# Kernel optimization log

Measured on AMD Instinct MI355X. Metric: run time of the kernel, lower is better.

Reference implementation:

```python
import jax, jax.numpy as jnp
import numpy as np

N = 30000        # nodes
E = 480000       # edges (before self-loops)
F_IN = 1280      # input_features
HID = 64         # hidden_dim
HEADS = 4
C = 2 * HID      # per-head GAT out channels (hidden_dim*2)
NEG_SLOPE = 0.2  # GATConv default negative_slope
EPS = 1e-5       # BatchNorm1d eps


def setup_inputs() -> dict:
    key = jax.random.key(0)
    ks = jax.random.split(key, 8)
    x = jax.random.normal(ks[0], (N, F_IN), jnp.float32)
    edge_index = jax.random.randint(ks[1], (2, E), 0, N)
    edge_weight = jax.random.uniform(ks[2], (E,), jnp.float32)
    W_gat = jax.random.normal(ks[3], (F_IN, HEADS * C), jnp.float32) / np.sqrt(F_IN)
    att_src = jax.random.normal(ks[4], (HEADS, C), jnp.float32) * 0.1
    att_dst = jax.random.normal(ks[5], (HEADS, C), jnp.float32) * 0.1
    b_gat = jnp.zeros((HEADS * C,), jnp.float32)
    bn_gamma = jnp.ones((HEADS * C,), jnp.float32)
    bn_beta = jnp.zeros((HEADS * C,), jnp.float32)
    W_gcn = jax.random.normal(ks[6], (HEADS * C, HID), jnp.float32) / np.sqrt(HEADS * C)
    b_gcn = jnp.zeros((HID,), jnp.float32)
    return dict(x=x, edge_index=edge_index, edge_weight=edge_weight, W_gat=W_gat,
                att_src=att_src, att_dst=att_dst, b_gat=b_gat, bn_gamma=bn_gamma,
                bn_beta=bn_beta, W_gcn=W_gcn, b_gcn=b_gcn)


def _segment_softmax(logits, seg, num):
    m = jax.ops.segment_max(logits, seg, num_segments=num)
    e = jnp.exp(logits - m[seg])
    s = jax.ops.segment_sum(e, seg, num_segments=num)
    return e / (s[seg] + 1e-16)


def reference(x, edge_index, edge_weight, W_gat, att_src, att_dst, b_gat,
              bn_gamma, bn_beta, W_gcn, b_gcn):
    n = x.shape[0]
    loops = jnp.arange(n)
    src = jnp.concatenate([edge_index[0], loops])  # self-loops added by both convs
    dst = jnp.concatenate([edge_index[1], loops])

    # ---- GATConv(F_IN -> HEADS*C, heads=4, concat) ----
    # (edge_weight plays no role: GATConv has edge_dim=None so edge_attr is unused)
    h = (x @ W_gat).reshape(n, HEADS, C)                  # [N,H,C]
    a_src = jnp.einsum('nhc,hc->nh', h, att_src)          # [N,H]
    a_dst = jnp.einsum('nhc,hc->nh', h, att_dst)
    logits = jax.nn.leaky_relu(a_src[src] + a_dst[dst], NEG_SLOPE)  # [E+N,H]
    alpha = _segment_softmax(logits, dst, n)              # softmax over incoming edges
    msg = h[src] * alpha[:, :, None]                      # [E+N,H,C]
    out1 = jax.ops.segment_sum(msg, dst, num_segments=n).reshape(n, HEADS * C) + b_gat

    # ---- BatchNorm1d (training-mode batch stats) + ReLU ----
    mean = out1.mean(axis=0)
    var = out1.var(axis=0)
    xr = jax.nn.relu((out1 - mean) * jax.lax.rsqrt(var + EPS) * bn_gamma + bn_beta)

    # ---- GCNConv(HEADS*C -> HID) with edge_weight, self-loops weight 1 ----
    w = jnp.concatenate([edge_weight, jnp.ones((n,), edge_weight.dtype)])
    deg = jax.ops.segment_sum(w, dst, num_segments=n)
    dinv = jnp.where(deg > 0, jax.lax.rsqrt(deg), 0.0)
    norm = dinv[src] * w * dinv[dst]                      # D^-1/2 A D^-1/2
    h2 = xr @ W_gcn                                       # [N,HID]
    out = jax.ops.segment_sum(h2[src] * norm[:, None], dst, num_segments=n) + b_gcn
    return out
```

## Files before the change

### kernel.cpp

```cpp
#include <hip/hip_runtime.h>
#include <hip/hip_bf16.h>
#include <math.h>

#define N_NODES 30000
#define N_EDGES 480000
#define EE_TOT  510000
#define F_INK   1280
#define HC      512
#define C_PH    128
#define NHID    64

typedef __attribute__((ext_vector_type(8))) short bf16x8;
typedef __attribute__((ext_vector_type(4))) float f32x4;

__device__ inline float wred_max(float v){
  #pragma unroll
  for (int o = 32; o; o >>= 1) v = fmaxf(v, __shfl_xor(v, o));
  return v;
}
__device__ inline float wred_sum(float v){
  #pragma unroll
  for (int o = 32; o; o >>= 1) v += __shfl_xor(v, o);
  return v;
}

__device__ __forceinline__ unsigned short f2bf(float f){
  unsigned u = __float_as_uint(f);
  unsigned r = (u + 0x7FFFu + ((u >> 16) & 1u)) >> 16;
  return (unsigned short)r;
}
__device__ __forceinline__ float b2f(unsigned short s){
  return __uint_as_float((unsigned)s << 16);
}

__device__ __forceinline__ void gld16(const void* g, void* l){
  __builtin_amdgcn_global_load_lds((const __attribute__((address_space(1))) unsigned int*)g,
                                   (__attribute__((address_space(3))) unsigned int*)l, 16, 0, 0);
}

__global__ __launch_bounds__(256) void cvtx(const float* __restrict__ x,
                                            unsigned short* __restrict__ xb){
  size_t i = ((size_t)blockIdx.x * 256 + threadIdx.x) * 4;
  float4 v = *(const float4*)&x[i];
  ushort4 o;
  o.x = f2bf(v.x); o.y = f2bf(v.y); o.z = f2bf(v.z); o.w = f2bf(v.w);
  *(ushort4*)&xb[i] = o;
}

__global__ __launch_bounds__(256) void cvtw(const float* __restrict__ W,
                                            unsigned short* __restrict__ Wb){
  __shared__ float tile[32][33];
  int tx = threadIdx.x & 31, ty = threadIdx.x >> 5;
  int n0 = blockIdx.x * 32, k0 = blockIdx.y * 32;
  #pragma unroll
  for (int i = 0; i < 4; i++){
    int r = ty + i * 8;
    tile[r][tx] = W[(size_t)(k0 + r) * HC + n0 + tx];
  }
  __syncthreads();
  #pragma unroll
  for (int i = 0; i < 4; i++){
    int r = ty + i * 8;
    Wb[(size_t)(n0 + r) * F_INK + k0 + tx] = f2bf(tile[tx][r]);
  }
}

__global__ __launch_bounds__(256) void cvtw2(const float* __restrict__ W,
                                             unsigned short* __restrict__ Wb){
  __shared__ float tile[32][33];
  int tx = threadIdx.x & 31, ty = threadIdx.x >> 5;
  int n0 = blockIdx.x * 32, k0 = blockIdx.y * 32;
  #pragma unroll
  for (int i = 0; i < 4; i++){
    int r = ty + i * 8;
    tile[r][tx] = W[(size_t)(k0 + r) * NHID + n0 + tx];
  }
  __syncthreads();
  #pragma unroll
  for (int i = 0; i < 4; i++){
    int r = ty + i * 8;
    Wb[(size_t)(n0 + r) * HC + k0 + tx] = f2bf(tile[tx][r]);
  }
}

#define BM 128
#define BK 32
#define KTILES (F_INK / BK)
__global__ __launch_bounds__(256) void gemm1_mfma(const unsigned short* __restrict__ A,
                                                  const unsigned short* __restrict__ B,
                                                  unsigned short* __restrict__ C){
  __shared__ __align__(16) unsigned short Ab[2][BM * BK];
  __shared__ __align__(16) unsigned short Bb[2][BM * BK];
  const int t = threadIdx.x, lane = t & 63, wid = t >> 6;
  const int wm = wid >> 1, wn = wid & 1;
  const int bm = blockIdx.y * BM, bn = blockIdx.x * BM;
  const int r15 = lane & 15;
  const int kq  = (lane >> 4) * 16;
  const int kqs = kq ^ (((r15 >> 1) & 3) << 4);
  const int srow  = (lane >> 2);
  const int skb   = ((lane & 3) * 16) ^ (((lane >> 3) & 3) << 4);

  f32x4 acc[4][4] = {};

  auto stage = [&](int buf, int kt){
    const int k0 = kt * BK;
    #pragma unroll
    for (int c = 0; c < 2; c++){
      int chunk = wid * 2 + c;
      int row = chunk * 16 + srow;
      int ar = bm + row; if (ar >= N_NODES) ar = N_NODES - 1;
      gld16(&A[(size_t)ar * F_INK + k0 + (skb >> 1)], &Ab[buf][chunk * 512]);
      gld16(&B[(size_t)(bn + row) * F_INK + k0 + (skb >> 1)], &Bb[buf][chunk * 512]);
    }
  };

  stage(0, 0);
  __syncthreads();

  for (int kt = 0; kt < KTILES; kt++){
    const int cur = kt & 1;
    if (kt + 1 < KTILES) stage(cur ^ 1, kt + 1);
    bf16x8 a[4], b[4];
    #pragma unroll
    for (int f = 0; f < 4; f++){
      int rowA = wm * 64 + f * 16 + r15;
      a[f] = *(const bf16x8*)((const char*)&Ab[cur][0] + rowA * 64 + kqs);
      int rowB = wn * 64 + f * 16 + r15;
      b[f] = *(const bf16x8*)((const char*)&Bb[cur][0] + rowB * 64 + kqs);
    }
    #pragma unroll
    for (int fm = 0; fm < 4; fm++)
      #pragma unroll
      for (int fn = 0; fn < 4; fn++)
        acc[fm][fn] = __builtin_amdgcn_mfma_f32_16x16x32_bf16(a[fm], b[fn], acc[fm][fn], 0, 0, 0);
    __syncthreads();
  }

  const int ccol0 = bn + wn * 64 + r15;
  #pragma unroll
  for (int fm = 0; fm < 4; fm++){
    #pragma unroll
    for (int j = 0; j < 4; j++){
      int row = bm + wm * 64 + fm * 16 + (lane >> 4) * 4 + j;
      if (row < N_NODES){
        #pragma unroll
        for (int fn = 0; fn < 4; fn++)
          C[(size_t)row * HC + ccol0 + fn * 16] = f2bf(acc[fm][fn][j]);
      }
    }
  }
}

__global__ __launch_bounds__(256) void attdot(const unsigned short* __restrict__ hb,
    const float* __restrict__ att_s, const float* __restrict__ att_d,
    float* __restrict__ a_src, float* __restrict__ a_dst){
  int n = blockIdx.x;
  int w = threadIdx.x >> 6;
  int lane = threadIdx.x & 63;
  const unsigned short* hr = hb + (size_t)n * HC + w * C_PH;
  ushort2 hv = *(const ushort2*)(hr + 2 * lane);
  float h0 = b2f(hv.x), h1 = b2f(hv.y);
  const float* as = att_s + w * C_PH;
  const float* ad = att_d + w * C_PH;
  float s1 = h0 * as[2*lane] + h1 * as[2*lane + 1];
  float s2 = h0 * ad[2*lane] + h1 * ad[2*lane + 1];
  s1 = wred_sum(s1); s2 = wred_sum(s2);
  if (lane == 0){ a_src[n*4 + w] = s1; a_dst[n*4 + w] = s2; }
}

__global__ void count_k(const int* __restrict__ ei, int* __restrict__ counts){
  int e = blockIdx.x * 256 + threadIdx.x;
  if (e >= EE_TOT) return;
  int d = (e < N_EDGES) ? ei[N_EDGES + e] : (e - N_EDGES);
  atomicAdd(&counts[d], 1);
}

__global__ __launch_bounds__(1024) void scan_k(const int* __restrict__ counts,
                                               int* __restrict__ offsets){
  __shared__ int sh[1024];
  int t = threadIdx.x;
  int base = t * 30;
  int tot = 0;
  for (int i = 0; i < 30; i++){
    int idx = base + i;
    tot += (idx < N_NODES) ? counts[idx] : 0;
  }
  sh[t] = tot; __syncthreads();
  for (int o = 1; o < 1024; o <<= 1){
    int v = (t >= o) ? sh[t - o] : 0;
    __syncthreads();
    sh[t] += v;
    __syncthreads();
  }
  int run = sh[t] - tot;
  for (int i = 0; i < 30; i++){
    int idx = base + i;
    if (idx < N_NODES){ offsets[idx] = run; run += counts[idx]; }
  }
  if (t == 1023) offsets[N_NODES] = sh[1023];
}

__global__ void fill_k(const int* __restrict__ ei, const float* __restrict__ ew,
                       int* __restrict__ cursor, const int* __restrict__ offsets,
                       int* __restrict__ src_s, float* __restrict__ w_s){
  int e = blockIdx.x * 256 + threadIdx.x;
  if (e >= EE_TOT) return;
  int s, d; float w;
  if (e < N_EDGES){ s = ei[e]; d = ei[N_EDGES + e]; w = ew[e]; }
  else            { s = d = e - N_EDGES; w = 1.0f; }
  int pos = offsets[d] + atomicAdd(&cursor[d], 1);
  src_s[pos] = s; w_s[pos] = w;
}

__global__ __launch_bounds__(64) void attnprep(const int* __restrict__ offsets,
    const int* __restrict__ src_s, const float* __restrict__ w_s,
    const float* __restrict__ a_src, const float* __restrict__ a_dst,
    float* __restrict__ alpha, float* __restrict__ dinv){
  int n = blockIdx.x, lane = threadIdx.x;
  int off = offsets[n], end = offsets[n + 1];
  float4 ad = *(const float4*)&a_dst[n * 4];
  float m0 = -1e30f, m1 = -1e30f, m2 = -1e30f, m3 = -1e30f;
  for (int i = off + lane; i < end; i += 64){
    int s = src_s[i];
    float4 as = *(const float4*)&a_src[s * 4];
    float l0 = as.x + ad.x; l0 = (l0 > 0.f) ? l0 : 0.2f * l0;
    float l1 = as.y + ad.y; l1 = (l1 > 0.f) ? l1 : 0.2f * l1;
    float l2 = as.z + ad.z; l2 = (l2 > 0.f) ? l2 : 0.2f * l2;
    float l3 = as.w + ad.w; l3 = (l3 > 0.f) ? l3 : 0.2f * l3;
    m0 = fmaxf(m0, l0); m1 = fmaxf(m1, l1); m2 = fmaxf(m2, l2); m3 = fmaxf(m3, l3);
  }
  m0 = wred_max(m0); m1 = wred_max(m1); m2 = wred_max(m2); m3 = wred_max(m3);
  float s0 = 0, s1 = 0, s2 = 0, s3 = 0, wsum = 0;
  for (int i = off + lane; i < end; i += 64){
    int s = src_s[i];
    float4 as = *(const float4*)&a_src[s * 4];
    float l0 = as.x + ad.x; l0 = (l0 > 0.f) ? l0 : 0.2f * l0;
    float l1 = as.y + ad.y; l1 = (l1 > 0.f) ? l1 : 0.2f * l1;
    float l2 = as.z + ad.z; l2 = (l2 > 0.f) ? l2 : 0.2f * l2;
    float l3 = as.w + ad.w; l3 = (l3 > 0.f) ? l3 : 0.2f * l3;
    float e0 = expf(l0 - m0), e1 = expf(l1 - m1), e2 = expf(l2 - m2), e3 = expf(l3 - m3);
    float4 av; av.x = e0; av.y = e1; av.z = e2; av.w = e3;
    *(float4*)&alpha[(size_t)i * 4] = av;
    s0 += e0; s1 += e1; s2 += e2; s3 += e3;
    wsum += w_s[i];
  }
  s0 = wred_sum(s0); s1 = wred_sum(s1); s2 = wred_sum(s2); s3 = wred_sum(s3);
  wsum = wred_sum(wsum);
  if (lane == 0) dinv[n] = (wsum > 0.f) ? rsqrtf(wsum) : 0.f;
  float r0 = 1.f / (s0 + 1e-16f), r1 = 1.f / (s1 + 1e-16f);
  float r2 = 1.f / (s2 + 1e-16f), r3 = 1.f / (s3 + 1e-16f);
  for (int i = off + lane; i < end; i += 64){
    float4 av = *(float4*)&alpha[(size_t)i * 4];
    av.x *= r0; av.y *= r1; av.z *= r2; av.w *= r3;
    *(float4*)&alpha[(size_t)i * 4] = av;
  }
}

__global__ __launch_bounds__(256) void gatagg(const int* __restrict__ offsets,
    const int* __restrict__ src_s, const float* __restrict__ alpha,
    const unsigned short* __restrict__ hb, const float* __restrict__ b_gat,
    float* __restrict__ out1){
  __shared__ int   s_l[64];
  __shared__ float a_s[64][4];
  int n = blockIdx.x, t = threadIdx.x, wid = t >> 6;
  int off = offsets[n], deg = offsets[n + 1] - off;
  float acc0 = 0, acc1 = 0;
  for (int done = 0; done < deg; done += 64){
    int ce = deg - done; if (ce > 64) ce = 64;
    __syncthreads();
    if (t < 64 && t < ce){
      int idx = off + done + t;
      s_l[t] = src_s[idx];
      float4 av = *(const float4*)&alpha[(size_t)idx * 4];
      a_s[t][0] = av.x; a_s[t][1] = av.y; a_s[t][2] = av.z; a_s[t][3] = av.w;
    }
    __syncthreads();
    for (int i = 0; i < ce; i++){
      const ushort2* hp = (const ushort2*)(hb + (size_t)s_l[i] * HC);
      ushort2 hv = hp[t];
      float a = a_s[i][wid];
      acc0 += b2f(hv.x) * a;
      acc1 += b2f(hv.y) * a;
    }
  }
  float2 o; o.x = acc0 + b_gat[2*t]; o.y = acc1 + b_gat[2*t + 1];
  *(float2*)&out1[(size_t)n * HC + 2*t] = o;
}

__global__ __launch_bounds__(256) void bnstats(const float* __restrict__ out1,
                                               float* __restrict__ bnacc){
  int t = threadIdx.x;
  float s1 = 0, q1 = 0, s2 = 0, q2 = 0;
  for (int n = blockIdx.x; n < N_NODES; n += gridDim.x){
    float v1 = out1[(size_t)n * HC + t];
    float v2 = out1[(size_t)n * HC + t + 256];
    s1 += v1; q1 += v1 * v1; s2 += v2; q2 += v2 * v2;
  }
  atomicAdd(&bnacc[t], s1);        atomicAdd(&bnacc[512 + t], q1);
  atomicAdd(&bnacc[t + 256], s2);  atomicAdd(&bnacc[512 + t + 256], q2);
}

__global__ void bnfinal(const float* __restrict__ bnacc, const float* __restrict__ gam,
                        const float* __restrict__ bet, float* __restrict__ bnp){
  int c = blockIdx.x * 256 + threadIdx.x;
  if (c >= 512) return;
  float mean = bnacc[c] * (1.0f / N_NODES);
  float var  = bnacc[512 + c] * (1.0f / N_NODES) - mean * mean;
  float sc = gam[c] * rsqrtf(var + 1e-5f);
  bnp[c] = sc;
  bnp[512 + c] = bet[c] - mean * sc;
}

__global__ __launch_bounds__(256) void bnprep(const float* __restrict__ out1,
    const float* __restrict__ bnp, unsigned short* __restrict__ xrb){
  size_t i = ((size_t)blockIdx.x * 256 + threadIdx.x) * 4;
  int c = (int)(i & (HC - 1));
  float4 v  = *(const float4*)&out1[i];
  float4 sc = *(const float4*)&bnp[c];
  float4 sh = *(const float4*)&bnp[512 + c];
  float r; ushort4 o;
  r = v.x * sc.x + sh.x; o.x = f2bf(r > 0.f ? r : 0.f);
  r = v.y * sc.y + sh.y; o.y = f2bf(r > 0.f ? r : 0.f);
  r = v.z * sc.z + sh.z; o.z = f2bf(r > 0.f ? r : 0.f);
  r = v.w * sc.w + sh.w; o.w = f2bf(r > 0.f ? r : 0.f);
  *(ushort4*)&xrb[i] = o;
}

#define BM2 128
#define BK2 32
__global__ __launch_bounds__(256) void gemm2_mfma(const unsigned short* __restrict__ A,
                                                  const unsigned short* __restrict__ B,
                                                  float* __restrict__ C){
  __shared__ __align__(16) unsigned short Ab[2][BM2 * BK2];
  __shared__ __align__(16) unsigned short Bb[2][NHID * BK2];
  const int t = threadIdx.x, lane = t & 63, wid = t >> 6;
  const int bm = blockIdx.x * BM2;
  const int r15 = lane & 15;
  const int kq  = (lane >> 4) * 16;
  const int kqs = kq ^ (((r15 >> 1) & 3) << 4);
  const int srow = lane >> 2;
  const int skb  = ((lane & 3) * 16) ^ (((lane >> 3) & 3) << 4);

  f32x4 acc[2][4] = {};

  auto stage = [&](int buf, int kt){
    const int k0 = kt * BK2;
    #pragma unroll
    for (int c = 0; c < 2; c++){
      int chunk = wid * 2 + c;
      int row = chunk * 16 + srow;
      int ar = bm + row; if (ar >= N_NODES) ar = N_NODES - 1;
      gld16(&A[(size_t)ar * HC + k0 + (skb >> 1)], &Ab[buf][chunk * 512]);
    }
    int rowB = wid * 16 + srow;
    gld16(&B[(size_t)rowB * HC + k0 + (skb >> 1)], &Bb[buf][wid * 512]);
  };

  stage(0, 0);
  __syncthreads();

  #pragma unroll 2
  for (int kt = 0; kt < HC / BK2; kt++){
    const int cur = kt & 1;
    if (kt + 1 < HC / BK2) stage(cur ^ 1, kt + 1);
    bf16x8 a[2], b[4];
    #pragma unroll
    for (int f = 0; f < 2; f++){
      int rowA = wid * 32 + f * 16 + r15;
      a[f] = *(const bf16x8*)((const char*)&Ab[cur][0] + rowA * 64 + kqs);
    }
    #pragma unroll
    for (int f = 0; f < 4; f++){
      int rowB = f * 16 + r15;
      b[f] = *(const bf16x8*)((const char*)&Bb[cur][0] + rowB * 64 + kqs);
    }
    #pragma unroll
    for (int fm = 0; fm < 2; fm++)
      #pragma unroll
      for (int fn = 0; fn < 4; fn++)
        acc[fm][fn] = __builtin_amdgcn_mfma_f32_16x16x32_bf16(a[fm], b[fn], acc[fm][fn], 0, 0, 0);
    __syncthreads();
  }

  #pragma unroll
  for (int fm = 0; fm < 2; fm++){
    #pragma unroll
    for (int j = 0; j < 4; j++){
      int row = bm + wid * 32 + fm * 16 + (lane >> 4) * 4 + j;
      if (row < N_NODES){
        #pragma unroll
        for (int fn = 0; fn < 4; fn++)
          C[(size_t)row * NHID + fn * 16 + r15] = acc[fm][fn][j];
      }
    }
  }
}

__global__ __launch_bounds__(64) void gcnagg(const int* __restrict__ offsets,
    const int* __restrict__ src_s, const float* __restrict__ w_s,
    const float* __restrict__ dinv, const float* __restrict__ h2,
    const float* __restrict__ b_gcn, float* __restrict__ out){
  int n = blockIdx.x, j = threadIdx.x;
  int off = offsets[n], end = offsets[n + 1];
  float dv = dinv[n];
  float acc = 0.f;
  for (int i = off; i < end; i++){
    int s = src_s[i];
    float nrm = dinv[s] * w_s[i] * dv;
    acc += h2[(size_t)s * NHID + j] * nrm;
  }
  out[(size_t)n * NHID + j] = acc + b_gcn[j];
}

extern "C" void kernel_launch(void* const* d_in, const int* in_sizes, int n_in,
                              void* d_out, int out_size, void* d_ws, size_t ws_size,
                              hipStream_t stream){
  const float* x    = (const float*)d_in[0];
  const int*   ei   = (const int*)d_in[1];
  const float* ew   = (const float*)d_in[2];
  const float* Wgat = (const float*)d_in[3];
  const float* atts = (const float*)d_in[4];
  const float* attd = (const float*)d_in[5];
  const float* bgat = (const float*)d_in[6];
  const float* gam  = (const float*)d_in[7];
  const float* bet  = (const float*)d_in[8];
  const float* Wgcn = (const float*)d_in[9];
  const float* bgcn = (const float*)d_in[10];
  float* out = (float*)d_out;

  char* ws = (char*)d_ws;
  size_t cur = 0;
  auto nb = [&](size_t bytes){ cur = (cur + 255) & ~(size_t)255; size_t r = cur; cur += bytes; return r; };
  int*   counts  = (int*)  (ws + nb((size_t)N_NODES * 4));
  int*   cursor  = (int*)  (ws + nb((size_t)N_NODES * 4));
  float* bnacc   = (float*)(ws + nb(1024 * 4));
  size_t zbytes  = cur;
  unsigned short* hb = (unsigned short*)(ws + nb((size_t)N_NODES * HC * 2));
  float* a_src   = (float*)(ws + nb((size_t)N_NODES * 4 * 4));
  float* a_dst   = (float*)(ws + nb((size_t)N_NODES * 4 * 4));
  int*   offsets = (int*)  (ws + nb((size_t)(N_NODES + 1) * 4));
  int*   src_s   = (int*)  (ws + nb((size_t)EE_TOT * 4));
  float* w_s     = (float*)(ws + nb((size_t)EE_TOT * 4));
  size_t reg0    = nb((size_t)EE_TOT * 16);
  size_t reg1    = nb((size_t)N_NODES * HC * 4);
  size_t reg2    = nb((size_t)N_NODES * NHID * 4);
  unsigned short* xb = (unsigned short*)(ws + reg0);
  float* alpha   = (float*)(ws + reg0);
  float* out1    = (float*)(ws + reg1);
  float* h2      = (float*)(ws + reg2);
  unsigned short* Wb  = (unsigned short*)(ws + nb((size_t)HC * F_INK * 2));
  unsigned short* Wtb = (unsigned short*)(ws + nb((size_t)NHID * HC * 2));
  unsigned short* xrb = (unsigned short*)(ws + nb((size_t)N_NODES * HC * 2));
  float* bnp     = (float*)(ws + nb(1024 * 4));
  float* dinvp   = (float*)(ws + nb((size_t)N_NODES * 4));
  (void)ws_size; (void)in_sizes; (void)n_in; (void)out_size;

  hipMemsetAsync(d_ws, 0, zbytes, stream);
  count_k <<<(EE_TOT + 255) / 256, 256, 0, stream>>>(ei, counts);
  scan_k  <<<1, 1024, 0, stream>>>(counts, offsets);
  fill_k  <<<(EE_TOT + 255) / 256, 256, 0, stream>>>(ei, ew, cursor, offsets, src_s, w_s);
  cvtx    <<<(N_NODES * F_INK / 4 + 255) / 256, 256, 0, stream>>>(x, xb);
  cvtw    <<<dim3(HC / 32, F_INK / 32), 256, 0, stream>>>(Wgat, Wb);
  cvtw2   <<<dim3(NHID / 32, HC / 32), 256, 0, stream>>>(Wgcn, Wtb);
  gemm1_mfma<<<dim3(HC / BM, (N_NODES + BM - 1) / BM), 256, 0, stream>>>(xb, Wb, hb);
  attdot  <<<N_NODES, 256, 0, stream>>>(hb, atts, attd, a_src, a_dst);
  attnprep<<<N_NODES, 64, 0, stream>>>(offsets, src_s, w_s, a_src, a_dst, alpha, dinvp);
  gatagg  <<<N_NODES, 256, 0, stream>>>(offsets, src_s, alpha, hb, bgat, out1);
  bnstats <<<256, 256, 0, stream>>>(out1, bnacc);
  bnfinal <<<2, 256, 0, stream>>>(bnacc, gam, bet, bnp);
  bnprep  <<<N_NODES * HC / 4 / 256, 256, 0, stream>>>(out1, bnp, xrb);
  gemm2_mfma<<<(N_NODES + BM2 - 1) / BM2, 256, 0, stream>>>(xrb, Wtb, h2);
  gcnagg  <<<N_NODES, 64, 0, stream>>>(offsets, src_s, w_s, dinvp, h2, bgcn, out);
}
```

Before: 629.0 us.

## Store GAT output in bf16 and retile GEMM1 to 64x256 blocks

The GAT aggregation output is now written as bf16 instead of fp32, and the batch-norm statistics and normalisation kernels read that bf16 buffer. This halves the traffic of the intermediate tensor. GEMM1 is retiled from 128x128 to 64x256 blocks, with each wave covering a full 64-row strip against its own 64-column slice. This reduces how often the larger A matrix is re-read across column blocks, at the cost of a smaller M tile. Rounding the pre-batch-norm activations to bf16 slightly reduces the precision of the statistics.

```diff
diff --git a/kernel.cpp b/kernel.cpp
--- a/kernel.cpp
+++ b/kernel.cpp
@@ -83,17 +83,17 @@
   }
 }
 
-#define BM 128
+#define BM1 64
+#define BN1 256
 #define BK 32
 #define KTILES (F_INK / BK)
 __global__ __launch_bounds__(256) void gemm1_mfma(const unsigned short* __restrict__ A,
                                                   const unsigned short* __restrict__ B,
                                                   unsigned short* __restrict__ C){
-  __shared__ __align__(16) unsigned short Ab[2][BM * BK];
-  __shared__ __align__(16) unsigned short Bb[2][BM * BK];
+  __shared__ __align__(16) unsigned short Ab[2][BM1 * BK];
+  __shared__ __align__(16) unsigned short Bb[2][BN1 * BK];
   const int t = threadIdx.x, lane = t & 63, wid = t >> 6;
-  const int wm = wid >> 1, wn = wid & 1;
-  const int bm = blockIdx.y * BM, bn = blockIdx.x * BM;
+  const int bm = blockIdx.y * BM1, bn = blockIdx.x * BN1;
   const int r15 = lane & 15;
   const int kq  = (lane >> 4) * 16;
   const int kqs = kq ^ (((r15 >> 1) & 3) << 4);
@@ -104,13 +104,15 @@
 
   auto stage = [&](int buf, int kt){
     const int k0 = kt * BK;
-    #pragma unroll
-    for (int c = 0; c < 2; c++){
-      int chunk = wid * 2 + c;
-      int row = chunk * 16 + srow;
+    {
+      int row = wid * 16 + srow;
       int ar = bm + row; if (ar >= N_NODES) ar = N_NODES - 1;
-      gld16(&A[(size_t)ar * F_INK + k0 + (skb >> 1)], &Ab[buf][chunk * 512]);
-      gld16(&B[(size_t)(bn + row) * F_INK + k0 + (skb >> 1)], &Bb[buf][chunk * 512]);
+      gld16(&A[(size_t)ar * F_INK + k0 + (skb >> 1)], &Ab[buf][wid * 512]);
+    }
+    #pragma unroll
+    for (int c = 0; c < 4; c++){
+      int ch = wid * 4 + c;
+      gld16(&B[(size_t)(bn + ch * 16 + srow) * F_INK + k0 + (skb >> 1)], &Bb[buf][ch * 512]);
     }
   };
 
@@ -123,9 +125,9 @@
     bf16x8 a[4], b[4];
     #pragma unroll
     for (int f = 0; f < 4; f++){
-      int rowA = wm * 64 + f * 16 + r15;
+      int rowA = f * 16 + r15;
       a[f] = *(const bf16x8*)((const char*)&Ab[cur][0] + rowA * 64 + kqs);
-      int rowB = wn * 64 + f * 16 + r15;
+      int rowB = wid * 64 + f * 16 + r15;
       b[f] = *(const bf16x8*)((const char*)&Bb[cur][0] + rowB * 64 + kqs);
     }
     #pragma unroll
@@ -136,12 +138,12 @@
     __syncthreads();
   }
 
-  const int ccol0 = bn + wn * 64 + r15;
+  const int ccol0 = bn + wid * 64 + r15;
   #pragma unroll
   for (int fm = 0; fm < 4; fm++){
     #pragma unroll
     for (int j = 0; j < 4; j++){
-      int row = bm + wm * 64 + fm * 16 + (lane >> 4) * 4 + j;
+      int row = bm + fm * 16 + (lane >> 4) * 4 + j;
       if (row < N_NODES){
         #pragma unroll
         for (int fn = 0; fn < 4; fn++)
@@ -259,7 +261,7 @@
 __global__ __launch_bounds__(256) void gatagg(const int* __restrict__ offsets,
     const int* __restrict__ src_s, const float* __restrict__ alpha,
     const unsigned short* __restrict__ hb, const float* __restrict__ b_gat,
-    float* __restrict__ out1){
+    unsigned short* __restrict__ out1b){
   __shared__ int   s_l[64];
   __shared__ float a_s[64][4];
   int n = blockIdx.x, t = threadIdx.x, wid = t >> 6;
@@ -283,21 +285,23 @@
       acc1 += b2f(hv.y) * a;
     }
   }
-  float2 o; o.x = acc0 + b_gat[2*t]; o.y = acc1 + b_gat[2*t + 1];
-  *(float2*)&out1[(size_t)n * HC + 2*t] = o;
-}
-
-__global__ __launch_bounds__(256) void bnstats(const float* __restrict__ out1,
+  ushort2 o;
+  o.x = f2bf(acc0 + b_gat[2*t]);
+  o.y = f2bf(acc1 + b_gat[2*t + 1]);
+  *(ushort2*)&out1b[(size_t)n * HC + 2*t] = o;
+}
+
+__global__ __launch_bounds__(256) void bnstats(const unsigned short* __restrict__ out1b,
                                                float* __restrict__ bnacc){
   int t = threadIdx.x;
   float s1 = 0, q1 = 0, s2 = 0, q2 = 0;
   for (int n = blockIdx.x; n < N_NODES; n += gridDim.x){
-    float v1 = out1[(size_t)n * HC + t];
-    float v2 = out1[(size_t)n * HC + t + 256];
+    ushort2 v = *(const ushort2*)&out1b[(size_t)n * HC + 2*t];
+    float v1 = b2f(v.x), v2 = b2f(v.y);
     s1 += v1; q1 += v1 * v1; s2 += v2; q2 += v2 * v2;
   }
-  atomicAdd(&bnacc[t], s1);        atomicAdd(&bnacc[512 + t], q1);
-  atomicAdd(&bnacc[t + 256], s2);  atomicAdd(&bnacc[512 + t + 256], q2);
+  atomicAdd(&bnacc[2*t], s1);      atomicAdd(&bnacc[512 + 2*t], q1);
+  atomicAdd(&bnacc[2*t + 1], s2);  atomicAdd(&bnacc[512 + 2*t + 1], q2);
 }
 
 __global__ void bnfinal(const float* __restrict__ bnacc, const float* __restrict__ gam,
@@ -311,18 +315,18 @@
   bnp[512 + c] = bet[c] - mean * sc;
 }
 
-__global__ __launch_bounds__(256) void bnprep(const float* __restrict__ out1,
+__global__ __launch_bounds__(256) void bnprep(const unsigned short* __restrict__ out1b,
     const float* __restrict__ bnp, unsigned short* __restrict__ xrb){
   size_t i = ((size_t)blockIdx.x * 256 + threadIdx.x) * 4;
   int c = (int)(i & (HC - 1));
-  float4 v  = *(const float4*)&out1[i];
+  ushort4 v4 = *(const ushort4*)&out1b[i];
   float4 sc = *(const float4*)&bnp[c];
   float4 sh = *(const float4*)&bnp[512 + c];
   float r; ushort4 o;
-  r = v.x * sc.x + sh.x; o.x = f2bf(r > 0.f ? r : 0.f);
-  r = v.y * sc.y + sh.y; o.y = f2bf(r > 0.f ? r : 0.f);
-  r = v.z * sc.z + sh.z; o.z = f2bf(r > 0.f ? r : 0.f);
-  r = v.w * sc.w + sh.w; o.w = f2bf(r > 0.f ? r : 0.f);
+  r = b2f(v4.x) * sc.x + sh.x; o.x = f2bf(r > 0.f ? r : 0.f);
+  r = b2f(v4.y) * sc.y + sh.y; o.y = f2bf(r > 0.f ? r : 0.f);
+  r = b2f(v4.z) * sc.z + sh.z; o.z = f2bf(r > 0.f ? r : 0.f);
+  r = b2f(v4.w) * sc.w + sh.w; o.w = f2bf(r > 0.f ? r : 0.f);
   *(ushort4*)&xrb[i] = o;
 }
 
@@ -446,7 +450,7 @@
   size_t reg2    = nb((size_t)N_NODES * NHID * 4);
   unsigned short* xb = (unsigned short*)(ws + reg0);
   float* alpha   = (float*)(ws + reg0);
-  float* out1    = (float*)(ws + reg1);
+  unsigned short* out1b = (unsigned short*)(ws + reg1);
   float* h2      = (float*)(ws + reg2);
   unsigned short* Wb  = (unsigned short*)(ws + nb((size_t)HC * F_INK * 2));
   unsigned short* Wtb = (unsigned short*)(ws + nb((size_t)NHID * HC * 2));
@@ -462,13 +466,13 @@
   cvtx    <<<(N_NODES * F_INK / 4 + 255) / 256, 256, 0, stream>>>(x, xb);
   cvtw    <<<dim3(HC / 32, F_INK / 32), 256, 0, stream>>>(Wgat, Wb);
   cvtw2   <<<dim3(NHID / 32, HC / 32), 256, 0, stream>>>(Wgcn, Wtb);
-  gemm1_mfma<<<dim3(HC / BM, (N_NODES + BM - 1) / BM), 256, 0, stream>>>(xb, Wb, hb);
+  gemm1_mfma<<<dim3(HC / BN1, (N_NODES + BM1 - 1) / BM1), 256, 0, stream>>>(xb, Wb, hb);
   attdot  <<<N_NODES, 256, 0, stream>>>(hb, atts, attd, a_src, a_dst);
   attnprep<<<N_NODES, 64, 0, stream>>>(offsets, src_s, w_s, a_src, a_dst, alpha, dinvp);
-  gatagg  <<<N_NODES, 256, 0, stream>>>(offsets, src_s, alpha, hb, bgat, out1);
-  bnstats <<<256, 256, 0, stream>>>(out1, bnacc);
+  gatagg  <<<N_NODES, 256, 0, stream>>>(offsets, src_s, alpha, hb, bgat, out1b);
+  bnstats <<<256, 256, 0, stream>>>(out1b, bnacc);
   bnfinal <<<2, 256, 0, stream>>>(bnacc, gam, bet, bnp);
-  bnprep  <<<N_NODES * HC / 4 / 256, 256, 0, stream>>>(out1, bnp, xrb);
+  bnprep  <<<N_NODES * HC / 4 / 256, 256, 0, stream>>>(out1b, bnp, xrb);
   gemm2_mfma<<<(N_NODES + BM2 - 1) / BM2, 256, 0, stream>>>(xrb, Wtb, h2);
   gcnagg  <<<N_NODES, 64, 0, stream>>>(offsets, src_s, w_s, dinvp, h2, bgcn, out);
 }
```

After: 624.3 us. About the same (-0.7%).
